# Kernel tuning notes

Measured on AMD Instinct MI355X. Metric: run time of the kernel, lower is better.

Reference implementation:

```python
import jax, jax.numpy as jnp
import numpy as np

V_PATCH_NUMS = (1, 2, 4, 6, 8, 10, 13, 16)
HW = 16
QUANT_RESI = 0.5
SHARE_K = 4
BETA = 1.0


def _pool_matrix(n_in, n_out):
    # adaptive average pooling as a [n_out, n_in] matrix (matches F.adaptive_avg_pool2d bins)
    P = np.zeros((n_out, n_in), np.float32)
    for i in range(n_out):
        s = (i * n_in) // n_out
        e = -((-(i + 1) * n_in) // n_out)  # ceil((i+1)*n_in/n_out)
        P[i, s:e] = 1.0 / (e - s)
    return jnp.asarray(P)


def _phi_index(si, SN):
    # PhiPartiallyShared.__getitem__(si/(SN-1)) with K=4 ticks
    K = SHARE_K
    ticks = np.linspace(1.0 / 3 / K, 1 - 1.0 / 3 / K, K) if K == 4 else np.linspace(1.0 / 2 / K, 1 - 1.0 / 2 / K, K)
    return int(np.argmin(np.abs(ticks - si / (SN - 1))))


def _phi(h, w, b):
    # Phi: h*(1-r) + conv3x3(h)*r, zero padding (nn.Conv2d default)
    y = jax.lax.conv_general_dilated(h, w, (1, 1), 'SAME',
                                     dimension_numbers=('NCHW', 'OIHW', 'NCHW'))
    y = y + b[None, :, None, None]
    return h * (1.0 - QUANT_RESI) + y * QUANT_RESI


def setup_inputs() -> dict:
    key = jax.random.key(0)
    k0, k1, k2 = jax.random.split(key, 3)
    B, C, V = 64, 32, 4096
    f = jax.random.normal(k0, (B, C, HW, HW), jnp.float32)
    embed = jax.random.normal(k1, (V, C), jnp.float32)  # EMAEmbedding.weight ~ randn
    phi_w = jax.random.normal(k2, (SHARE_K, C, C, 3, 3), jnp.float32) * (1.0 / np.sqrt(9.0 * C))
    phi_b = jnp.zeros((SHARE_K, C), jnp.float32)
    return {"f_BChw": f, "embed_weight": embed, "phi_w": phi_w, "phi_b": phi_b}


def reference(f_BChw, embed_weight, phi_w, phi_b):
    B, C, H, W = f_BChw.shape
    SN = len(V_PATCH_NUMS)
    f_ng = jax.lax.stop_gradient(f_BChw)
    f_hat = jnp.zeros_like(f_BChw)
    e_sq = jnp.sum(embed_weight * embed_weight, axis=1)  # [V]
    loss = jnp.float32(0.0)
    for si, pn in enumerate(V_PATCH_NUMS):
        rest = f_ng - jax.lax.stop_gradient(f_hat)  # residual to quantize (no grad through distance)
        if pn != H:
            P = _pool_matrix(H, pn)
            rest_d = jnp.einsum('oh,bchw,pw->bcop', P, rest, P)  # adaptive avg pool -> [B,C,pn,pn]
        else:
            rest_d = rest
        rest_NC = rest_d.transpose(0, 2, 3, 1).reshape(-1, C)  # [B*pn*pn, C]
        # squared euclidean cdist to codebook, argmin
        d = (jnp.sum(rest_NC * rest_NC, axis=1, keepdims=True)
             + e_sq[None, :]
             - 2.0 * (rest_NC @ embed_weight.T))  # [N, V]
        idx = jnp.argmin(d, axis=1)  # [B*pn*pn] int
        h = embed_weight[idx].reshape(B, pn, pn, C).transpose(0, 3, 1, 2)  # gather -> [B,C,pn,pn]
        if pn != H:
            h = jax.image.resize(h, (B, C, H, W), method='linear')  # bilinear, align_corners=False
        k = _phi_index(si, SN)
        h = _phi(h, phi_w[k], phi_b[k])
        f_hat = f_hat + h
        loss = loss + 0.25 * jnp.mean((jax.lax.stop_gradient(f_hat) - f_BChw) ** 2) \
                    + BETA * jnp.mean((f_hat - f_ng) ** 2)
    loss = loss / SN
    # straight-through estimator: grads flow to f_BChw as identity
    f_hat_st = jax.lax.stop_gradient(f_hat - f_BChw) + f_BChw
    return f_hat_st, loss
```

## Files before the change

kernel.cpp:

```cpp
#include <hip/hip_runtime.h>
#include <hip/hip_bf16.h>

#define BB 64
#define CC 32
#define HW2 256
#define VV 4096
#define NELEM (BB*CC*HW2)
#define PADW 18
#define PADA 324

#define OFF_F     0
#define OFF_FHAT  (OFF_F     + NELEM)
#define OFF_EMBT  (OFF_FHAT  + NELEM)
#define OFF_ESQ   (OFF_EMBT  + VV*CC)
#define OFF_PW    (OFF_ESQ   + VV)
#define OFF_PB    (OFF_PW    + 4*CC*CC*9)
#define OFF_REST  (OFF_PB    + 4*CC)
#define OFF_BESTA (OFF_REST  + 16384*CC)
#define OFF_BESTB (OFF_BESTA + 2*16384)
#define OFF_LOSS  (OFF_BESTB + 2*16384)
#define OFF_FLAG  (OFF_LOSS  + 1)
#define OFF_EMBR  (OFF_FLAG  + 1)
#define WS_NEED_EMBR ((OFF_EMBR + VV*CC) * 4)

__device__ __forceinline__ int embt_idx(int v, int c) {
    return (v >> 6) * 2048 + c * 64 + (v & 63);
}

__global__ void k_probe(const void* __restrict__ fin, int* __restrict__ flag) {
    __shared__ int cnt[256];
    int t = threadIdx.x;
    const __hip_bfloat16* p = (const __hip_bfloat16*)fin;
    int local = 0;
    for (int i = t; i < 8192; i += 256) {
        float v = __bfloat162float(p[i]);
        if (!(fabsf(v) < 1e3f)) local++;
    }
    cnt[t] = local;
    __syncthreads();
    for (int s = 128; s > 0; s >>= 1) {
        if (t < s) cnt[t] += cnt[t + s];
        __syncthreads();
    }
    if (t == 0) *flag = (cnt[0] >= 64) ? 1 : 0;
}

__global__ void k_prep(const void* __restrict__ fin,
                       const void* __restrict__ ein,
                       const void* __restrict__ win,
                       const void* __restrict__ bin_,
                       const int* __restrict__ flag,
                       float* __restrict__ f, float* __restrict__ fhat,
                       float* __restrict__ embT, float* __restrict__ pw,
                       float* __restrict__ pb, float* __restrict__ loss,
                       float* __restrict__ embR, int use_embR) {
    bool isf32 = (*flag != 0);
    int i = blockIdx.x * 256 + threadIdx.x;
    if (i < NELEM) {
        f[i] = isf32 ? ((const float*)fin)[i]
                     : __bfloat162float(((const __hip_bfloat16*)fin)[i]);
        fhat[i] = 0.f;
    }
    if (i < VV*CC) {
        float ev = isf32 ? ((const float*)ein)[i]
                         : __bfloat162float(((const __hip_bfloat16*)ein)[i]);
        int v = i >> 5, c = i & 31;
        embT[embt_idx(v, c)] = ev;
        if (use_embR) embR[i] = ev;
    }
    if (i < 4*CC*CC*9)
        pw[i] = isf32 ? ((const float*)win)[i]
                      : __bfloat162float(((const __hip_bfloat16*)win)[i]);
    if (i < 4*CC)
        pb[i] = isf32 ? ((const float*)bin_)[i]
                      : __bfloat162float(((const __hip_bfloat16*)bin_)[i]);
    if (i == 0) *loss = 0.f;
}

__global__ void k_esq(const float* __restrict__ embT, float* __restrict__ esq) {
    int v = blockIdx.x * 256 + threadIdx.x;
    if (v >= VV) return;
    const float* p = embT + (v >> 6) * 2048 + (v & 63);
    float s = 0.f;
    #pragma unroll
    for (int c = 0; c < CC; ++c) { float e = p[c * 64]; s = fmaf(e, e, s); }
    esq[v] = s;
}

__global__ void k_pool0(const float* __restrict__ f, const float* __restrict__ fhat,
                        float* __restrict__ rest, unsigned long long* __restrict__ best) {
    int n = threadIdx.x;
    int c = blockIdx.y;
    if (n >= BB) return;
    if (c == 0) best[n] = 0xFFFFFFFFFFFFFFFFull;
    const float* fb = f + (n * CC + c) * HW2;
    const float* hb = fhat + (n * CC + c) * HW2;
    float s = 0.f;
    for (int h = 0; h < 16; ++h)
        for (int w = 0; w < 16; ++w)
            s += fb[h * 16 + w] - hb[h * 16 + w];
    rest[n * CC + c] = s * (1.f / 256.f);
}

__global__ __launch_bounds__(256, 3)
void k_argmin_big(const float* __restrict__ rest, const float* __restrict__ embT,
                  const float* __restrict__ esq, unsigned long long* __restrict__ best,
                  int Ntot, int cpw) {
    __shared__ float xT[CC][132];
    __shared__ float eT[2 * CC * 64];
    __shared__ float xxs[2][128];
    int tid = threadIdx.x;
    int tx = tid & 15, ty = tid >> 4;
    int qblk = blockIdx.x * 128;
    int v0 = blockIdx.y * cpw;
    int t0 = v0 >> 6;

    {
        int q = tid >> 1, h = tid & 1;
        int qq = qblk + q; if (qq > Ntot - 1) qq = Ntot - 1;
        const float* xr = rest + qq * CC + h * 16;
        float part = 0.f;
        #pragma unroll
        for (int c = 0; c < 16; ++c) {
            float xv = xr[c];
            xT[h * 16 + c][q] = xv;
            part = fmaf(xv, xv, part);
        }
        xxs[h][q] = part;
    }
    __syncthreads();

    float xx[8];
    #pragma unroll
    for (int i = 0; i < 8; ++i) {
        int q = (i >> 2) * 64 + ty * 4 + (i & 3);
        xx[i] = xxs[0][q] + xxs[1][q];
    }

    float bd[8]; int bi[8];
    #pragma unroll
    for (int i = 0; i < 8; ++i) { bd[i] = 3.4e38f; bi[i] = v0; }

    int ntiles = cpw >> 7;
    for (int t = 0; t < ntiles; ++t) {
        int vbase = v0 + t * 128;
        const float* gt = embT + (size_t)(t0 + 2 * t) * 2048;
        float4 s0 = *(const float4*)(gt + tid * 4);
        float4 s1 = *(const float4*)(gt + 1024 + tid * 4);
        float4 s2 = *(const float4*)(gt + 2048 + tid * 4);
        float4 s3 = *(const float4*)(gt + 3072 + tid * 4);
        __syncthreads();
        *(float4*)(eT + tid * 4) = s0;
        *(float4*)(eT + 1024 + tid * 4) = s1;
        *(float4*)(eT + 2048 + tid * 4) = s2;
        *(float4*)(eT + 3072 + tid * 4) = s3;
        __syncthreads();

        float acc[8][8];
        #pragma unroll
        for (int i = 0; i < 8; ++i)
            #pragma unroll
            for (int j = 0; j < 8; ++j) acc[i][j] = 0.f;

        #pragma unroll 8
        for (int k = 0; k < CC; ++k) {
            float4 a0 = *(const float4*)&xT[k][ty * 4];
            float4 a1 = *(const float4*)&xT[k][64 + ty * 4];
            float4 b0 = *(const float4*)(eT + k * 64 + tx * 4);
            float4 b1 = *(const float4*)(eT + 2048 + k * 64 + tx * 4);
            float a[8] = {a0.x, a0.y, a0.z, a0.w, a1.x, a1.y, a1.z, a1.w};
            float b[8] = {b0.x, b0.y, b0.z, b0.w, b1.x, b1.y, b1.z, b1.w};
            #pragma unroll
            for (int i = 0; i < 8; ++i)
                #pragma unroll
                for (int j = 0; j < 8; ++j)
                    acc[i][j] = fmaf(a[i], b[j], acc[i][j]);
        }

        float4 e0 = *(const float4*)(esq + vbase + tx * 4);
        float4 e1 = *(const float4*)(esq + vbase + 64 + tx * 4);
        float es[8] = {e0.x, e0.y, e0.z, e0.w, e1.x, e1.y, e1.z, e1.w};
        #pragma unroll
        for (int i = 0; i < 8; ++i) {
            float base = xx[i];
            #pragma unroll
            for (int j = 0; j < 8; ++j) {
                float dist = fmaf(-2.f, acc[i][j], base + es[j]);
                int vidx = vbase + (j >> 2) * 64 + tx * 4 + (j & 3);
                if (dist < bd[i]) { bd[i] = dist; bi[i] = vidx; }
            }
        }
    }

    #pragma unroll
    for (int i = 0; i < 8; ++i) {
        unsigned u = __float_as_uint(bd[i]);
        unsigned long long mono = (u & 0x80000000u)
            ? (unsigned long long)(~u)
            : (unsigned long long)(u | 0x80000000u);
        unsigned long long pk = (mono << 32) | (unsigned long long)(unsigned)bi[i];
        #pragma unroll
        for (int m = 1; m <= 8; m <<= 1) {
            unsigned long long o = __shfl_xor(pk, m, 64);
            if (o < pk) pk = o;
        }
        int q = qblk + (i >> 2) * 64 + ty * 4 + (i & 3);
        if (tx == 0 && q < Ntot)
            atomicMin(best + q, pk);
    }
}

__global__ __launch_bounds__(256, 4)
void k_argmin_small(const float* __restrict__ rest, const float* __restrict__ embT,
                    const float* __restrict__ esq, unsigned long long* __restrict__ best,
                    int Ntot, int cpw) {
    int tid  = threadIdx.x;
    int w    = tid >> 6, lane = tid & 63;
    int q0   = blockIdx.x * 512 + w * 128 + lane;
    int q1   = q0 + 64;
    int v0   = blockIdx.y * cpw;

    bool act0 = (q0 < Ntot), act1 = (q1 < Ntot);
    if (!act0 && !act1) return;
    int qa = act0 ? q0 : (Ntot - 1);
    int qb = act1 ? q1 : (Ntot - 1);

    float a0v[32], a1v[32];
    {
        const float4* ra = (const float4*)(rest + qa * CC);
        const float4* rb = (const float4*)(rest + qb * CC);
        #pragma unroll
        for (int c4 = 0; c4 < 8; ++c4) {
            float4 va = ra[c4], vb4 = rb[c4];
            a0v[c4*4+0] = va.x;  a0v[c4*4+1] = va.y;
            a0v[c4*4+2] = va.z;  a0v[c4*4+3] = va.w;
            a1v[c4*4+0] = vb4.x; a1v[c4*4+1] = vb4.y;
            a1v[c4*4+2] = vb4.z; a1v[c4*4+3] = vb4.w;
        }
    }

    float p0a = 0.f, p1a = 0.f, p0b = 0.f, p1b = 0.f;
    #pragma unroll
    for (int c = 0; c < 16; ++c)  p0a = fmaf(a0v[c], a0v[c], p0a);
    #pragma unroll
    for (int c = 16; c < 32; ++c) p1a = fmaf(a0v[c], a0v[c], p1a);
    #pragma unroll
    for (int c = 0; c < 16; ++c)  p0b = fmaf(a1v[c], a1v[c], p0b);
    #pragma unroll
    for (int c = 16; c < 32; ++c) p1b = fmaf(a1v[c], a1v[c], p1b);
    float xx0 = p0a + p1a;
    float xx1 = p0b + p1b;

    float bd0 = 3.4e38f, bd1 = 3.4e38f;
    int   bi0 = v0,      bi1 = v0;

    int ntiles = cpw >> 3;
    for (int t = 0; t < ntiles; ++t) {
        int vb = v0 + t * 8;
        int boff = __builtin_amdgcn_readfirstlane((vb >> 6) * 2048 + (vb & 63));
        int eoff = __builtin_amdgcn_readfirstlane(vb);
        const float* bt = embT + boff;
        const float* ep = esq + eoff;

        float acc0[8], acc1[8];
        #pragma unroll
        for (int j = 0; j < 8; ++j) { acc0[j] = 0.f; acc1[j] = 0.f; }

        #pragma unroll
        for (int k = 0; k < CC; ++k) {
            float a0 = a0v[k], a1 = a1v[k];
            #pragma unroll
            for (int j = 0; j < 8; ++j) {
                float bv = bt[k * 64 + j];
                acc0[j] = fmaf(a0, bv, acc0[j]);
                acc1[j] = fmaf(a1, bv, acc1[j]);
            }
        }

        #pragma unroll
        for (int j = 0; j < 8; ++j) {
            float es = ep[j];
            float d0 = fmaf(-2.f, acc0[j], xx0 + es);
            if (d0 < bd0) { bd0 = d0; bi0 = vb + j; }
            float d1 = fmaf(-2.f, acc1[j], xx1 + es);
            if (d1 < bd1) { bd1 = d1; bi1 = vb + j; }
        }
    }

    unsigned u0 = __float_as_uint(bd0);
    unsigned long long mono0 = (u0 & 0x80000000u)
        ? (unsigned long long)(~u0)
        : (unsigned long long)(u0 | 0x80000000u);
    unsigned long long pk0 = (mono0 << 32) | (unsigned long long)(unsigned)bi0;
    unsigned u1 = __float_as_uint(bd1);
    unsigned long long mono1 = (u1 & 0x80000000u)
        ? (unsigned long long)(~u1)
        : (unsigned long long)(u1 | 0x80000000u);
    unsigned long long pk1 = (mono1 << 32) | (unsigned long long)(unsigned)bi1;

    if (act0) atomicMin(best + q0, pk0);
    if (act1) atomicMin(best + q1, pk1);
}

__global__ __launch_bounds__(256)
void k_fuse(const float* __restrict__ embT,
            const unsigned long long* __restrict__ best,
            const float* __restrict__ pw, const float* __restrict__ pb,
            const float* __restrict__ f, float* __restrict__ fhat,
            float* __restrict__ loss,
            float* __restrict__ rest,
            unsigned long long* __restrict__ best_next,
            const float* __restrict__ embR,
            int pn, int k, int pn_next) {
    __shared__ float h_pad[CC * PADA];
    __shared__ float extra[CC * 169];
    __shared__ float red[4];
    int b = blockIdx.x, co8 = blockIdx.y, t = threadIdx.x;
    int nn = pn * pn;
    int y = t >> 4, x = t & 15;

    for (int i = t; i < CC * PADA; i += 256) h_pad[i] = 0.f;

    if (pn == 16) {
        __syncthreads();
        int id = (int)(unsigned)(best[b * HW2 + t] & 0xFFFFFFFFull);
        int ctr = (y + 1) * PADW + (x + 1);
        if (embR) {
            const float4* er4 = (const float4*)(embR + id * CC);
            #pragma unroll
            for (int c4 = 0; c4 < 8; ++c4) {
                float4 v = er4[c4];
                h_pad[(c4*4+0) * PADA + ctr] = v.x;
                h_pad[(c4*4+1) * PADA + ctr] = v.y;
                h_pad[(c4*4+2) * PADA + ctr] = v.z;
                h_pad[(c4*4+3) * PADA + ctr] = v.w;
            }
        } else {
            const float* er = embT + (id >> 6) * 2048 + (id & 63);
            #pragma unroll
            for (int c = 0; c < CC; ++c)
                h_pad[c * PADA + ctr] = er[c * 64];
        }
    } else {
        float (*hs)[169] = (float(*)[169])extra;
        for (int cell = t; cell < nn; cell += 256) {
            int id = (int)(unsigned)(best[b * nn + cell] & 0xFFFFFFFFull);
            if (embR) {
                const float4* er4 = (const float4*)(embR + id * CC);
                #pragma unroll
                for (int c4 = 0; c4 < 8; ++c4) {
                    float4 v = er4[c4];
                    hs[c4*4+0][cell] = v.x;
                    hs[c4*4+1][cell] = v.y;
                    hs[c4*4+2][cell] = v.z;
                    hs[c4*4+3][cell] = v.w;
                }
            } else {
                const float* er = embT + (id >> 6) * 2048 + (id & 63);
                #pragma unroll
                for (int c = 0; c < CC; ++c) hs[c][cell] = er[c * 64];
            }
        }
        __syncthreads();
        float scale = (float)pn / 16.f;
        float sy = (y + 0.5f) * scale - 0.5f;
        sy = fminf(fmaxf(sy, 0.f), (float)(pn - 1));
        int y0 = (int)sy; int y1 = min(y0 + 1, pn - 1); float wy = sy - (float)y0;
        float sx = (x + 0.5f) * scale - 0.5f;
        sx = fminf(fmaxf(sx, 0.f), (float)(pn - 1));
        int x0 = (int)sx; int x1 = min(x0 + 1, pn - 1); float wx = sx - (float)x0;
        float wy0 = 1.f - wy, wx0 = 1.f - wx;
        int ctr = (y + 1) * PADW + (x + 1);
        #pragma unroll
        for (int c = 0; c < CC; ++c) {
            float v00 = hs[c][y0 * pn + x0], v01 = hs[c][y0 * pn + x1];
            float v10 = hs[c][y1 * pn + x0], v11 = hs[c][y1 * pn + x1];
            float a0 = wy0 * v00 + wy * v10;
            float a1 = wy0 * v01 + wy * v11;
            h_pad[c * PADA + ctr] = wx0 * a0 + wx * a1;
        }
    }
    __syncthreads();

    float acc[8];
    #pragma unroll
    for (int o = 0; o < 8; ++o) acc[o] = 0.f;
    const float* hbase = h_pad + y * PADW + x;
    const float* wpk = pw + (k * CC + co8 * 8) * (CC * 9);
    #pragma unroll
    for (int ci_ = 0; ci_ < CC; ++ci_) {
        float hv[9];
        #pragma unroll
        for (int dy = 0; dy < 3; ++dy)
            #pragma unroll
            for (int dx = 0; dx < 3; ++dx)
                hv[dy * 3 + dx] = hbase[ci_ * PADA + dy * PADW + dx];
        const float* wp = wpk + ci_ * 9;
        #pragma unroll
        for (int o = 0; o < 8; ++o) {
            const float* w9 = wp + o * (CC * 9);
            #pragma unroll
            for (int q = 0; q < 9; ++q) acc[o] = fmaf(hv[q], w9[q], acc[o]);
        }
    }

    float* diff = extra;
    float lsum = 0.f;
    int ctr = (y + 1) * PADW + (x + 1);
    #pragma unroll
    for (int o = 0; o < 8; ++o) {
        int co = co8 * 8 + o;
        float hval = h_pad[co * PADA + ctr];
        float outv = hval * 0.5f + (acc[o] + pb[k * CC + co]) * 0.5f;
        int pos = (b * CC + co) * HW2 + t;
        float fh = fhat[pos] + outv;
        fhat[pos] = fh;
        float dd = f[pos] - fh;
        diff[o * HW2 + t] = dd;
        lsum = fmaf(dd, dd, lsum);
    }
    #pragma unroll
    for (int off = 32; off > 0; off >>= 1) lsum += __shfl_down(lsum, off, 64);
    if ((t & 63) == 0) red[t >> 6] = lsum;
    __syncthreads();
    if (t == 0)
        atomicAdd(loss, red[0] + red[1] + red[2] + red[3]);

    if (pn_next > 0) {
        int nn2 = pn_next * pn_next;
        for (int q = t; q < nn2 * 8; q += 256) {
            int cell = q % nn2, o = q / nn2;
            int i = cell / pn_next, j = cell % pn_next;
            int s0 = (i * 16) / pn_next, e0 = ((i + 1) * 16 + pn_next - 1) / pn_next;
            int s1 = (j * 16) / pn_next, e1 = ((j + 1) * 16 + pn_next - 1) / pn_next;
            float inv = 1.f / (float)((e0 - s0) * (e1 - s1));
            float s = 0.f;
            for (int h = s0; h < e0; ++h)
                for (int w = s1; w < e1; ++w)
                    s += diff[o * HW2 + h * 16 + w];
            rest[(b * nn2 + cell) * CC + co8 * 8 + o] = s * inv;
        }
        if (co8 == 0)
            for (int q = t; q < nn2; q += 256)
                best_next[b * nn2 + q] = 0xFFFFFFFFFFFFFFFFull;
    }
}

__global__ void k_out(const float* __restrict__ fhat, const float* __restrict__ loss,
                      const int* __restrict__ flag, void* __restrict__ out) {
    bool isf32 = (*flag != 0);
    int i = blockIdx.x * 256 + threadIdx.x;
    if (i > NELEM) return;
    float v;
    if (i < NELEM) v = fhat[i];
    else           v = (*loss) * (1.25f / (float)NELEM / 8.f);
    if (isf32) ((float*)out)[i] = v;
    else       ((__hip_bfloat16*)out)[i] = __float2bfloat16(v);
}

extern "C" void kernel_launch(void* const* d_in, const int* in_sizes, int n_in,
                              void* d_out, int out_size, void* d_ws, size_t ws_size,
                              hipStream_t stream) {
    const void* fin  = d_in[0];
    const void* ein  = d_in[1];
    const void* win  = d_in[2];
    const void* bin_ = d_in[3];
    float* ws = (float*)d_ws;
    float* f    = ws + OFF_F;
    float* fhat = ws + OFF_FHAT;
    float* embT = ws + OFF_EMBT;
    float* esq  = ws + OFF_ESQ;
    float* pw   = ws + OFF_PW;
    float* pb   = ws + OFF_PB;
    float* rest = ws + OFF_REST;
    unsigned long long* bestA = (unsigned long long*)(ws + OFF_BESTA);
    unsigned long long* bestB = (unsigned long long*)(ws + OFF_BESTB);
    float* loss = ws + OFF_LOSS;
    int*   flag = (int*)(ws + OFF_FLAG);
    int use_embR = (ws_size >= (size_t)WS_NEED_EMBR) ? 1 : 0;
    float* embR = use_embR ? (ws + OFF_EMBR) : nullptr;

    static const int PN[8] = {1, 2, 4, 6, 8, 10, 13, 16};
    static const int KK[8] = {0, 0, 1, 1, 2, 2, 3, 3};
    static const int SPs[4] = {512, 512, 512, 256};
    static const int SPb[4] = {16, 16, 8, 8};

    k_probe<<<1, 256, 0, stream>>>(fin, flag);
    k_prep<<<(NELEM + 255) / 256, 256, 0, stream>>>(fin, ein, win, bin_, flag,
                                                    f, fhat, embT, pw, pb, loss,
                                                    embR, use_embR);
    k_esq<<<(VV + 255) / 256, 256, 0, stream>>>(embT, esq);
    k_pool0<<<dim3(1, CC), 256, 0, stream>>>(f, fhat, rest, bestA);

    for (int si = 0; si < 8; ++si) {
        int pn = PN[si];
        int Ntot = BB * pn * pn;
        unsigned long long* bcur = (si & 1) ? bestB : bestA;
        unsigned long long* bnxt = (si & 1) ? bestA : bestB;
        int pn_next = (si < 7) ? PN[si + 1] : 0;
        if (si < 4) {
            int Sp = SPs[si];
            int cpw = VV / Sp;
            int gx = (Ntot + 511) / 512;
            k_argmin_small<<<dim3(gx, Sp), 256, 0, stream>>>(rest, embT, esq, bcur,
                                                             Ntot, cpw);
        } else {
            int Sp = SPb[si - 4];
            int cpw = VV / Sp;
            int gx = (Ntot + 127) / 128;
            k_argmin_big<<<dim3(gx, Sp), 256, 0, stream>>>(rest, embT, esq, bcur,
                                                           Ntot, cpw);
        }
        k_fuse<<<dim3(BB, 4), 256, 0, stream>>>(embT, bcur, pw, pb, f, fhat, loss,
                                                rest, bnxt, embR, pn, KK[si], pn_next);
    }
    k_out<<<(NELEM + 1 + 255) / 256, 256, 0, stream>>>(fhat, loss, flag, d_out);
}
```

Before: 486.9 us.

## Retile phi conv in fuse kernel: 2 pixels x 2 channels per thread, 8 channel groups

The 3x3 conv in the fused kernel is remapped so each thread computes two adjacent pixels for two output channels, using float2 shared-memory window loads and wave-uniform weight addressing via readfirstlane. The grid doubles to 8 channel groups of 4, which halves per-block conv work and raises block count. Only the padding border of the shared halo buffer is zeroed instead of the whole buffer, and one barrier is dropped. The trade-off is that each block redundantly rebuilds the full upsampled h tile for fewer output channels.

```diff
diff --git a/kernel.cpp b/kernel.cpp
--- a/kernel.cpp
+++ b/kernel.cpp
@@ -319,10 +319,17 @@
     int nn = pn * pn;
     int y = t >> 4, x = t & 15;
 
-    for (int i = t; i < CC * PADA; i += 256) h_pad[i] = 0.f;
+    for (int i = t; i < CC * 68; i += 256) {
+        int c = i / 68, cell = i % 68;
+        int yy, xx;
+        if (cell < 18)      { yy = 0;  xx = cell; }
+        else if (cell < 36) { yy = 17; xx = cell - 18; }
+        else if (cell < 52) { yy = cell - 36 + 1; xx = 0; }
+        else                { yy = cell - 52 + 1; xx = 17; }
+        h_pad[c * PADA + yy * PADW + xx] = 0.f;
+    }
 
     if (pn == 16) {
-        __syncthreads();
         int id = (int)(unsigned)(best[b * HW2 + t] & 0xFFFFFFFFull);
         int ctr = (y + 1) * PADW + (x + 1);
         if (embR) {
@@ -382,42 +389,66 @@
     }
     __syncthreads();
 
-    float acc[8];
-    #pragma unroll
-    for (int o = 0; o < 8; ++o) acc[o] = 0.f;
-    const float* hbase = h_pad + y * PADW + x;
-    const float* wpk = pw + (k * CC + co8 * 8) * (CC * 9);
+    int wv  = t >> 6, lane = t & 63;
+    int cg  = wv & 1;
+    int pg  = (wv >> 1) * 64 + lane;
+    int cy  = pg >> 3, cx0 = (pg & 7) * 2;
+    int cob = co8 * 4 + cg * 2;
+    int wuni = __builtin_amdgcn_readfirstlane(k * CC + cob);
+    const float* wpk = pw + wuni * (CC * 9);
+
+    float acc00 = 0.f, acc01 = 0.f, acc10 = 0.f, acc11 = 0.f;
+    const float* hb0 = h_pad + cy * PADW + cx0;
     #pragma unroll
     for (int ci_ = 0; ci_ < CC; ++ci_) {
-        float hv[9];
-        #pragma unroll
-        for (int dy = 0; dy < 3; ++dy)
-            #pragma unroll
-            for (int dx = 0; dx < 3; ++dx)
-                hv[dy * 3 + dx] = hbase[ci_ * PADA + dy * PADW + dx];
-        const float* wp = wpk + ci_ * 9;
-        #pragma unroll
-        for (int o = 0; o < 8; ++o) {
-            const float* w9 = wp + o * (CC * 9);
-            #pragma unroll
-            for (int q = 0; q < 9; ++q) acc[o] = fmaf(hv[q], w9[q], acc[o]);
+        float win[3][4];
+        #pragma unroll
+        for (int dy = 0; dy < 3; ++dy) {
+            float2 r0 = *(const float2*)(hb0 + ci_ * PADA + dy * PADW);
+            float2 r1 = *(const float2*)(hb0 + ci_ * PADA + dy * PADW + 2);
+            win[dy][0] = r0.x; win[dy][1] = r0.y;
+            win[dy][2] = r1.x; win[dy][3] = r1.y;
+        }
+        const float* w0 = wpk + ci_ * 9;
+        const float* w1 = wpk + CC * 9 + ci_ * 9;
+        #pragma unroll
+        for (int q = 0; q < 9; ++q) {
+            int dy = q / 3, dx = q % 3;
+            float wv0 = w0[q], wv1 = w1[q];
+            acc00 = fmaf(win[dy][dx],     wv0, acc00);
+            acc01 = fmaf(win[dy][dx],     wv1, acc01);
+            acc10 = fmaf(win[dy][dx + 1], wv0, acc10);
+            acc11 = fmaf(win[dy][dx + 1], wv1, acc11);
         }
     }
 
     float* diff = extra;
     float lsum = 0.f;
-    int ctr = (y + 1) * PADW + (x + 1);
-    #pragma unroll
-    for (int o = 0; o < 8; ++o) {
-        int co = co8 * 8 + o;
-        float hval = h_pad[co * PADA + ctr];
-        float outv = hval * 0.5f + (acc[o] + pb[k * CC + co]) * 0.5f;
-        int pos = (b * CC + co) * HW2 + t;
-        float fh = fhat[pos] + outv;
-        fhat[pos] = fh;
-        float dd = f[pos] - fh;
-        diff[o * HW2 + t] = dd;
-        lsum = fmaf(dd, dd, lsum);
+    {
+        int ctrc = (cy + 1) * PADW + (cx0 + 1);
+        #pragma unroll
+        for (int oo = 0; oo < 2; ++oo) {
+            int co = cob + oo;
+            float bias = pb[k * CC + co];
+            float a0 = oo ? acc01 : acc00;
+            float a1 = oo ? acc11 : acc10;
+            int pos = (b * CC + co) * HW2 + cy * 16 + cx0;
+            float2 fh2 = *(float2*)(fhat + pos);
+            float2 f2  = *(const float2*)(f + pos);
+            float hv0 = h_pad[co * PADA + ctrc];
+            float hv1 = h_pad[co * PADA + ctrc + 1];
+            float out0 = hv0 * 0.5f + (a0 + bias) * 0.5f;
+            float out1 = hv1 * 0.5f + (a1 + bias) * 0.5f;
+            fh2.x += out0; fh2.y += out1;
+            *(float2*)(fhat + pos) = fh2;
+            float dd0 = f2.x - fh2.x;
+            float dd1 = f2.y - fh2.y;
+            int dbase = (cg * 2 + oo) * HW2 + cy * 16 + cx0;
+            diff[dbase]     = dd0;
+            diff[dbase + 1] = dd1;
+            lsum = fmaf(dd0, dd0, lsum);
+            lsum = fmaf(dd1, dd1, lsum);
+        }
     }
     #pragma unroll
     for (int off = 32; off > 0; off >>= 1) lsum += __shfl_down(lsum, off, 64);
@@ -428,7 +459,7 @@
 
     if (pn_next > 0) {
         int nn2 = pn_next * pn_next;
-        for (int q = t; q < nn2 * 8; q += 256) {
+        for (int q = t; q < nn2 * 4; q += 256) {
             int cell = q % nn2, o = q / nn2;
             int i = cell / pn_next, j = cell % pn_next;
             int s0 = (i * 16) / pn_next, e0 = ((i + 1) * 16 + pn_next - 1) / pn_next;
@@ -438,7 +469,7 @@
             for (int h = s0; h < e0; ++h)
                 for (int w = s1; w < e1; ++w)
                     s += diff[o * HW2 + h * 16 + w];
-            rest[(b * nn2 + cell) * CC + co8 * 8 + o] = s * inv;
+            rest[(b * nn2 + cell) * CC + co8 * 4 + o] = s * inv;
         }
         if (co8 == 0)
             for (int q = t; q < nn2; q += 256)
@@ -511,7 +542,7 @@
             k_argmin_big<<<dim3(gx, Sp), 256, 0, stream>>>(rest, embT, esq, bcur,
                                                            Ntot, cpw);
         }
-        k_fuse<<<dim3(BB, 4), 256, 0, stream>>>(embT, bcur, pw, pb, f, fhat, loss,
+        k_fuse<<<dim3(BB, 8), 256, 0, stream>>>(embT, bcur, pw, pb, f, fhat, loss,
                                                 rest, bnxt, embR, pn, KK[si], pn_next);
     }
     k_out<<<(NELEM + 1 + 255) / 256, 256, 0, stream>>>(fhat, loss, flag, d_out);
```

Measured after the change: 449.3 us (median of 2 runs). -7.7%, faster.
